# Optimization experiments

Hardware: AMD Instinct MI355X
Metric: run time of the kernel (lower is better)

Reference implementation:

```python
import jax, jax.numpy as jnp
import numpy as np

EMB = 256
HID = 512
VOCAB = 32000
SRC_LEN = 50
TRG_LEN = 50
BATCH = 64


def lstm_layer(x, h0, c0, Wih, Whh, b):
    """x: [T,B,in]; h0,c0: [B,H]; Wih: [4H,in]; Whh: [4H,H]; b: [4H].
    PyTorch gate order i,f,g,o. Returns (ys [T,B,H], hT, cT)."""
    def step(carry, xt):
        h, c = carry
        g = xt @ Wih.T + h @ Whh.T + b
        i, f, gg, o = jnp.split(g, 4, axis=-1)
        c = jax.nn.sigmoid(f) * c + jax.nn.sigmoid(i) * jnp.tanh(gg)
        h = jax.nn.sigmoid(o) * jnp.tanh(c)
        return (h, c), h
    (hT, cT), ys = jax.lax.scan(step, (h0, c0), x)
    return ys, hT, cT


def setup_inputs() -> dict:
    key = jax.random.key(0)
    ks = jax.random.split(key, 20)
    s = 0.05
    d = {
        'src': jax.random.randint(ks[0], (SRC_LEN, BATCH), 0, VOCAB),
        'trg': jax.random.randint(ks[1], (TRG_LEN, BATCH), 0, VOCAB),
        'enc_emb': jax.random.normal(ks[2], (VOCAB, EMB), jnp.float32) * s,
        'enc_Wih0': jax.random.normal(ks[3], (4 * HID, EMB), jnp.float32) * s,
        'enc_Whh0': jax.random.normal(ks[4], (4 * HID, HID), jnp.float32) * s,
        'enc_b0': jnp.zeros((4 * HID,), jnp.float32),
        'enc_Wih1': jax.random.normal(ks[5], (4 * HID, HID), jnp.float32) * s,
        'enc_Whh1': jax.random.normal(ks[6], (4 * HID, HID), jnp.float32) * s,
        'enc_b1': jnp.zeros((4 * HID,), jnp.float32),
        'dec_emb': jax.random.normal(ks[7], (VOCAB, EMB), jnp.float32) * s,
        'dec_Wih0': jax.random.normal(ks[8], (4 * HID, EMB), jnp.float32) * s,
        'dec_Whh0': jax.random.normal(ks[9], (4 * HID, HID), jnp.float32) * s,
        'dec_b0': jnp.zeros((4 * HID,), jnp.float32),
        'dec_Wih1': jax.random.normal(ks[10], (4 * HID, HID), jnp.float32) * s,
        'dec_Whh1': jax.random.normal(ks[11], (4 * HID, HID), jnp.float32) * s,
        'dec_b1': jnp.zeros((4 * HID,), jnp.float32),
        'out_W': jax.random.normal(ks[12], (VOCAB, HID), jnp.float32) * s,
        'out_b': jnp.zeros((VOCAB,), jnp.float32),
    }
    return d


def reference(src, trg, enc_emb, enc_Wih0, enc_Whh0, enc_b0, enc_Wih1, enc_Whh1,
              enc_b1, dec_emb, dec_Wih0, dec_Whh0, dec_b0, dec_Wih1, dec_Whh1,
              dec_b1, out_W, out_b):
    B = src.shape[1]
    z = jnp.zeros((B, HID), enc_emb.dtype)
    # Encoder: 2-layer LSTM over src, keep final (h, c) per layer
    xe = enc_emb[src]                                   # [S,B,E]
    y0, h0, c0 = lstm_layer(xe, z, z, enc_Wih0, enc_Whh0, enc_b0)
    _, h1, c1 = lstm_layer(y0, z, z, enc_Wih1, enc_Whh1, enc_b1)
    # Decoder with teacher forcing: inputs are trg[0:T-1]
    xd = dec_emb[trg[:-1]]                              # [T-1,B,E]
    d0, _, _ = lstm_layer(xd, h0, c0, dec_Wih0, dec_Whh0, dec_b0)
    d1, _, _ = lstm_layer(d0, h1, c1, dec_Wih1, dec_Whh1, dec_b1)
    preds = d1 @ out_W.T + out_b                        # [T-1,B,V]
    return preds
```

## Files before the change

kernel.cpp:

```cpp
#include <hip/hip_runtime.h>
#include <hip/hip_bf16.h>

#define BATCH 64
#define HID 512
#define EMB 256
#define VOCAB 32000
#define G4 2048

typedef __attribute__((ext_vector_type(8))) short short8;
typedef __attribute__((ext_vector_type(4))) float f32x4;
typedef __attribute__((ext_vector_type(4))) unsigned short ush4;

__global__ __launch_bounds__(256) void zero_kernel(float* p, int n){
    int i = blockIdx.x*256 + threadIdx.x;
    if (i < n) p[i] = 0.f;
}

__global__ __launch_bounds__(256) void embed_kernel(const int* __restrict__ tok,
                                                    const float* __restrict__ emb,
                                                    float* __restrict__ out, int T){
    int i = blockIdx.x*256 + threadIdx.x;
    int n = T*BATCH*(EMB/4);
    if (i >= n) return;
    int e4 = i % (EMB/4);
    int tb = i / (EMB/4);
    int id = tok[tb];
    reinterpret_cast<float4*>(out)[(size_t)tb*(EMB/4) + e4] =
        reinterpret_cast<const float4*>(emb + (size_t)id*EMB)[e4];
}

__device__ __forceinline__ unsigned short bf16_rne(float x){
    unsigned b = __float_as_uint(x);
    return (unsigned short)((b + 0x7fffu + ((b >> 16) & 1u)) >> 16);
}
__device__ __forceinline__ void split2(float x, unsigned short& h, unsigned short& l){
    h = bf16_rne(x);
    l = bf16_rne(x - __uint_as_float((unsigned)h << 16));
}

__global__ __launch_bounds__(256) void split_kernel(const float* __restrict__ in,
                                                    unsigned short* __restrict__ hi,
                                                    unsigned short* __restrict__ lo, int n4){
    int i = blockIdx.x*256 + threadIdx.x;
    if (i >= n4) return;
    f32x4 v = reinterpret_cast<const f32x4*>(in)[i];
    ush4 h, l;
    #pragma unroll
    for (int j = 0; j < 4; j++){ unsigned short a,b; split2(v[j], a, b); h[j]=a; l[j]=b; }
    reinterpret_cast<ush4*>(hi)[i] = h;
    reinterpret_cast<ush4*>(lo)[i] = l;
}

__global__ __launch_bounds__(256) void split_hi_kernel(const float* __restrict__ in,
                                                       unsigned short* __restrict__ hi, int n4){
    int i = blockIdx.x*256 + threadIdx.x;
    if (i >= n4) return;
    f32x4 v = reinterpret_cast<const f32x4*>(in)[i];
    ush4 h;
    #pragma unroll
    for (int j = 0; j < 4; j++) h[j] = bf16_rne(v[j]);
    reinterpret_cast<ush4*>(hi)[i] = h;
}

template<int KDIM, int NDIM>
__global__ __launch_bounds__(256) void gemm_mfma_split(
    const float* __restrict__ A, const float* __restrict__ B,
    const float* __restrict__ bias, float* __restrict__ C, int M)
{
    constexpr int LS = 40;
    __shared__ unsigned short Ah[128*LS], Al[128*LS], Bh[128*LS], Bl[128*LS];
    const int n0 = blockIdx.x*128, m0 = blockIdx.y*128;
    const int tid  = threadIdx.x;
    const int lane = tid & 63, wid = tid >> 6;
    const int wm = wid >> 1, wn = wid & 1;
    const int srow = tid >> 1, sk = (tid & 1)*16;
    f32x4 acc[4][4] = {};

    for (int k0 = 0; k0 < KDIM; k0 += 32){
        __syncthreads();
        {
            int ar = m0 + srow;
            float xv[16];
            if (ar < M){
                const float4* ap = reinterpret_cast<const float4*>(A + (size_t)ar*KDIM + k0 + sk);
                #pragma unroll
                for (int q = 0; q < 4; q++){
                    float4 v = ap[q];
                    xv[q*4+0]=v.x; xv[q*4+1]=v.y; xv[q*4+2]=v.z; xv[q*4+3]=v.w;
                }
            } else {
                #pragma unroll
                for (int q = 0; q < 16; q++) xv[q] = 0.f;
            }
            #pragma unroll
            for (int q = 0; q < 16; q++){
                unsigned short h,l; split2(xv[q], h, l);
                Ah[srow*LS + sk + q] = h;
                Al[srow*LS + sk + q] = l;
            }
        }
        {
            int br = n0 + srow;
            const float4* bp = reinterpret_cast<const float4*>(B + (size_t)br*KDIM + k0 + sk);
            #pragma unroll
            for (int q = 0; q < 4; q++){
                float4 v = bp[q];
                float xs[4] = {v.x, v.y, v.z, v.w};
                #pragma unroll
                for (int j = 0; j < 4; j++){
                    unsigned short h,l; split2(xs[j], h, l);
                    Bh[srow*LS + sk + q*4 + j] = h;
                    Bl[srow*LS + sk + q*4 + j] = l;
                }
            }
        }
        __syncthreads();
        const int fr = lane & 15, fk = (lane >> 4)*8;
        short8 a_h[4], a_l[4], b_h[4], b_l[4];
        #pragma unroll
        for (int mi = 0; mi < 4; mi++){
            int row = wm*64 + mi*16 + fr;
            a_h[mi] = *reinterpret_cast<const short8*>(&Ah[row*LS + fk]);
            a_l[mi] = *reinterpret_cast<const short8*>(&Al[row*LS + fk]);
        }
        #pragma unroll
        for (int nj = 0; nj < 4; nj++){
            int rowb = wn*64 + nj*16 + fr;
            b_h[nj] = *reinterpret_cast<const short8*>(&Bh[rowb*LS + fk]);
            b_l[nj] = *reinterpret_cast<const short8*>(&Bl[rowb*LS + fk]);
        }
        #pragma unroll
        for (int mi = 0; mi < 4; mi++)
            #pragma unroll
            for (int nj = 0; nj < 4; nj++){
                acc[mi][nj] = __builtin_amdgcn_mfma_f32_16x16x32_bf16(a_h[mi], b_h[nj], acc[mi][nj], 0,0,0);
                acc[mi][nj] = __builtin_amdgcn_mfma_f32_16x16x32_bf16(a_h[mi], b_l[nj], acc[mi][nj], 0,0,0);
                acc[mi][nj] = __builtin_amdgcn_mfma_f32_16x16x32_bf16(a_l[mi], b_h[nj], acc[mi][nj], 0,0,0);
            }
    }
    const int fr = lane & 15, fq = lane >> 4;
    #pragma unroll
    for (int nj = 0; nj < 4; nj++){
        int col = n0 + wn*64 + nj*16 + fr;
        float bv = bias[col];
        #pragma unroll
        for (int mi = 0; mi < 4; mi++){
            int rbase = m0 + wm*64 + mi*16 + fq*4;
            #pragma unroll
            for (int j = 0; j < 4; j++){
                int row = rbase + j;
                if (row < M)
                    __builtin_nontemporal_store(acc[mi][nj][j] + bv, &C[(size_t)row*NDIM + col]);
            }
        }
    }
}

__device__ __forceinline__ void gll16(const unsigned short* g, unsigned short* l){
    __builtin_amdgcn_global_load_lds(
        (const __attribute__((address_space(1))) unsigned int*)g,
        (__attribute__((address_space(3))) unsigned int*)l, 16, 0, 0);
}

template<int KDIM, int NDIM, int NTN, int PASSES>
__global__ __launch_bounds__(256) void gemm_planes_gll(
    const unsigned short* __restrict__ Ahi, const unsigned short* __restrict__ Alo,
    const unsigned short* __restrict__ Bhi, const unsigned short* __restrict__ Blo,
    const float* __restrict__ bias, float* __restrict__ C, int M)
{
    constexpr int NP = (PASSES == 3) ? 4 : 3;
    __shared__ unsigned short P[NP][128*32];
    const int total = gridDim.x;
    const int q = total >> 3, r8 = total & 7;
    const int xcd = blockIdx.x & 7, idx = blockIdx.x >> 3;
    const int lid = (xcd < r8 ? xcd*(q+1) : r8*(q+1) + (xcd - r8)*q) + idx;
    const int m0 = (lid / NTN)*128, n0 = (lid % NTN)*128;

    const int tid  = threadIdx.x;
    const int lane = tid & 63, wid = tid >> 6;
    const int wm = wid >> 1, wn = wid & 1;

    const bool stager = (PASSES == 3) || (wid < 3);
    const unsigned short* gsrc = (wid == 0) ? Ahi : (wid == 1) ? Alo
                               : (wid == 2) ? Bhi : Blo;
    const int row0 = (wid < 2) ? m0 : n0;
    const unsigned short* gbase = gsrc + (size_t)(row0 + (lane >> 2))*KDIM
                                       + 8*((lane & 3) ^ ((lane >> 3) & 3));
    unsigned short* lbase = &P[(wid < NP) ? wid : 0][0];

    f32x4 acc[4][4] = {};

    for (int k0 = 0; k0 < KDIM; k0 += 32){
        __syncthreads();
        if (stager){
            #pragma unroll
            for (int i = 0; i < 8; i++)
                gll16(gbase + k0 + (size_t)i*16*KDIM, lbase + i*512);
        }
        __syncthreads();

        const int fr = lane & 15, fkq = lane >> 4;
        const int swz = 8*(fkq ^ ((fr >> 1) & 3));
        short8 a_h[4], a_l[4], b_h[4], b_l[4];
        #pragma unroll
        for (int mi = 0; mi < 4; mi++){
            int row = wm*64 + mi*16 + fr;
            a_h[mi] = *reinterpret_cast<const short8*>(&P[0][row*32 + swz]);
            a_l[mi] = *reinterpret_cast<const short8*>(&P[1][row*32 + swz]);
        }
        #pragma unroll
        for (int nj = 0; nj < 4; nj++){
            int row = wn*64 + nj*16 + fr;
            b_h[nj] = *reinterpret_cast<const short8*>(&P[2][row*32 + swz]);
            if (PASSES == 3)
                b_l[nj] = *reinterpret_cast<const short8*>(&P[NP-1][row*32 + swz]);
        }
        #pragma unroll
        for (int mi = 0; mi < 4; mi++)
            #pragma unroll
            for (int nj = 0; nj < 4; nj++){
                acc[mi][nj] = __builtin_amdgcn_mfma_f32_16x16x32_bf16(a_h[mi], b_h[nj], acc[mi][nj], 0,0,0);
                acc[mi][nj] = __builtin_amdgcn_mfma_f32_16x16x32_bf16(a_l[mi], b_h[nj], acc[mi][nj], 0,0,0);
                if (PASSES == 3)
                    acc[mi][nj] = __builtin_amdgcn_mfma_f32_16x16x32_bf16(a_h[mi], b_l[nj], acc[mi][nj], 0,0,0);
            }
    }
    const int fr = lane & 15, fq = lane >> 4;
    #pragma unroll
    for (int nj = 0; nj < 4; nj++){
        int col = n0 + wn*64 + nj*16 + fr;
        float bv = bias[col];
        #pragma unroll
        for (int mi = 0; mi < 4; mi++){
            int rbase = m0 + wm*64 + mi*16 + fq*4;
            #pragma unroll
            for (int j = 0; j < 4; j++){
                int row = rbase + j;
                if (row < M)
                    __builtin_nontemporal_store(acc[mi][nj][j] + bv, &C[(size_t)row*NDIM + col]);
            }
        }
    }
}

__device__ __forceinline__ void lstm_body(
    const float* __restrict__ Xp, const float* __restrict__ Whh,
    const float* __restrict__ hinit, const float* __restrict__ cinit,
    float* __restrict__ ys, float* __restrict__ cfin,
    int T, unsigned* __restrict__ flagbase, int bx)
{
    constexpr int WS = 520;
    __shared__ unsigned short hH[8*WS], hL[8*WS];
    __shared__ float red[2048 + 128];
    __shared__ unsigned short zbuf[8];

    const int hc  = bx & 31, bc = bx >> 5;
    const int hid0 = hc*16;
    const int tid = threadIdx.x;
    const int lane = tid & 63, kc = tid >> 6;
    const int fr = lane & 15, fkq = lane >> 4;
    unsigned* myflag = flagbase + (size_t)(bc*32 + hc)*16;

    if (tid < 8) zbuf[tid] = 0;

    short8 ah[4][4], al[4][4];
    #pragma unroll
    for (int m = 0; m < 4; m++){
        const float* wr = Whh + (size_t)(m*HID + hid0 + fr)*HID;
        #pragma unroll
        for (int s = 0; s < 4; s++){
            int k0 = kc*128 + s*32 + fkq*8;
            f32x4 v0 = *reinterpret_cast<const f32x4*>(wr + k0);
            f32x4 v1 = *reinterpret_cast<const f32x4*>(wr + k0 + 4);
            short8 h8, l8;
            float xv[8] = {v0[0],v0[1],v0[2],v0[3],v1[0],v1[1],v1[2],v1[3]};
            #pragma unroll
            for (int j = 0; j < 8; j++){
                unsigned short hh, ll; split2(xv[j], hh, ll);
                h8[j] = (short)hh; l8[j] = (short)ll;
            }
            ah[m][s] = h8; al[m][s] = l8;
        }
    }

    const int ub = tid >> 4;
    const int uh = tid & 15;
    float creg = 0.f;
    if (tid < 128) creg = cinit[(size_t)(bc*8 + ub)*HID + hid0 + uh];

    const size_t hbase = (size_t)bc*8*HID;
    const float* xprow = Xp + (size_t)(bc*8 + ub)*G4 + hid0 + uh;

    float xn0=0.f, xn1=0.f, xn2=0.f, xn3=0.f;
    if (tid < 128){
        const float* xpr = xprow;
        xn0 = xpr[0]; xn1 = xpr[512]; xn2 = xpr[1024]; xn3 = xpr[1536];
    }

    for (int t = 0; t < T; t++){
        {
            const f32x4* hsrc = reinterpret_cast<const f32x4*>(
                (t == 0) ? (hinit + hbase) : (ys + (size_t)(t-1)*BATCH*HID + hbase));
            #pragma unroll
            for (int j = 0; j < 4; j++){
                int fidx = tid + j*256;
                f32x4 v = hsrc[fidx];
                int e   = fidx*4;
                int row = e >> 9, col = e & 511;
                ush4 h, l;
                #pragma unroll
                for (int qq = 0; qq < 4; qq++){ unsigned short a,b; split2(v[qq], a, b); h[qq]=a; l[qq]=b; }
                *reinterpret_cast<ush4*>(&hH[row*WS + col]) = h;
                *reinterpret_cast<ush4*>(&hL[row*WS + col]) = l;
            }
        }
        __syncthreads();

        {
            f32x4 acc4[4] = {};
            const bool breal = fr < 8;
            #pragma unroll
            for (int s = 0; s < 4; s++){
                int k0 = kc*128 + s*32 + fkq*8;
                short8 bh = breal ? *reinterpret_cast<const short8*>(&hH[fr*WS + k0])
                                  : *reinterpret_cast<const short8*>(zbuf);
                short8 bl = breal ? *reinterpret_cast<const short8*>(&hL[fr*WS + k0])
                                  : *reinterpret_cast<const short8*>(zbuf);
                #pragma unroll
                for (int m = 0; m < 4; m++){
                    acc4[m] = __builtin_amdgcn_mfma_f32_16x16x32_bf16(ah[m][s], bh, acc4[m], 0,0,0);
                    acc4[m] = __builtin_amdgcn_mfma_f32_16x16x32_bf16(ah[m][s], bl, acc4[m], 0,0,0);
                    acc4[m] = __builtin_amdgcn_mfma_f32_16x16x32_bf16(al[m][s], bh, acc4[m], 0,0,0);
                }
            }
            const int b = lane & 15;
            if (b < 8){
                #pragma unroll
                for (int m = 0; m < 4; m++)
                    #pragma unroll
                    for (int qq = 0; qq < 4; qq++){
                        int rowp = m*16 + (lane >> 4)*4 + qq;
                        red[kc*512 + rowp*8 + b] = acc4[m][qq];
                    }
            }
        }
        __syncthreads();

        if (tid < 64){
            #pragma unroll
            for (int b = 0; b < 8; b++)
                red[tid*8 + b] = red[tid*8 + b] + red[512 + tid*8 + b]
                               + red[1024 + tid*8 + b] + red[1536 + tid*8 + b];
        }
        __syncthreads();

        if (tid < 128){
            float gi = red[(0*16 + uh)*8 + ub] + xn0;
            float gf = red[(1*16 + uh)*8 + ub] + xn1;
            float gg = red[(2*16 + uh)*8 + ub] + xn2;
            float go = red[(3*16 + uh)*8 + ub] + xn3;
            float si = 1.f/(1.f + expf(-gi));
            float sf = 1.f/(1.f + expf(-gf));
            float so = 1.f/(1.f + expf(-go));
            float tg = tanhf(gg);
            float c = sf*creg + si*tg;
            creg = c;
            red[2048 + tid] = so * tanhf(c);
            if (t < T-1){
                const float* xpr = xprow + (size_t)(t+1)*BATCH*G4;
                xn0 = xpr[0]; xn1 = xpr[512]; xn2 = xpr[1024]; xn3 = xpr[1536];
            }
        }
        __syncthreads();

        if (tid < 64){
            if (tid < 32){
                f32x4 v = *reinterpret_cast<const f32x4*>(&red[2048 + tid*4]);
                const f32x4* addr = reinterpret_cast<const f32x4*>(
                    ys + (size_t)t*BATCH*HID
                       + (size_t)(bc*8 + (tid >> 2))*HID + hid0 + (tid & 3)*4);
                asm volatile("global_store_dwordx4 %0, %1, off sc0 sc1"
                             :: "v"(addr), "v"(v) : "memory");
            }
            if (t < T-1){
                asm volatile("s_waitcnt vmcnt(0)" ::: "memory");
                if (tid == 0)
                    __hip_atomic_store(myflag, (unsigned)(t+1),
                                       __ATOMIC_RELAXED, __HIP_MEMORY_SCOPE_AGENT);
                const unsigned tgt = (unsigned)(t+1);
                unsigned* fp = flagbase + (size_t)(bc*32 + (tid & 31))*16;
                unsigned spins = 0;
                bool done = false;
                while (!done && spins < (1u<<20)){
                    unsigned v = tgt;
                    if (tid < 32)
                        v = __hip_atomic_load(fp, __ATOMIC_RELAXED, __HIP_MEMORY_SCOPE_AGENT);
                    done = (bool)__all((int)(v >= tgt));
                    spins++;
                }
            }
        }
        __syncthreads();
    }

    if (tid < 128)
        cfin[(size_t)(bc*8 + ub)*HID + hid0 + uh] = creg;
}

__global__ __launch_bounds__(256, 2) void lstm_layer_k(
    const float* Xp, const float* Whh, const float* hinit, const float* cinit,
    float* ys, float* cfin, int T, unsigned* flagbase)
{
    lstm_body(Xp, Whh, hinit, cinit, ys, cfin, T, flagbase, blockIdx.x);
}

__global__ __launch_bounds__(256, 2) void lstm_dual_k(
    const float* Xp0, const float* Whh0, const float* hi0, const float* ci0,
    float* ys0, float* cf0, int T0, unsigned* fl0,
    const float* Xp1, const float* Whh1, const float* hi1, const float* ci1,
    float* ys1, float* cf1, int T1, unsigned* fl1)
{
    const int role = blockIdx.x >> 8;
    const int bx = blockIdx.x & 255;
    const float* Xp   = role ? Xp1 : Xp0;
    const float* Whh  = role ? Whh1 : Whh0;
    const float* hi   = role ? hi1 : hi0;
    const float* ci   = role ? ci1 : ci0;
    float* ys         = role ? ys1 : ys0;
    float* cf         = role ? cf1 : cf0;
    int T             = role ? T1 : T0;
    unsigned* fl      = role ? fl1 : fl0;
    lstm_body(Xp, Whh, hi, ci, ys, cf, T, fl, bx);
}

extern "C" void kernel_launch(void* const* d_in, const int* in_sizes, int n_in,
                              void* d_out, int out_size, void* d_ws, size_t ws_size,
                              hipStream_t stream) {
    const int*   src      = (const int*)  d_in[0];
    const int*   trg      = (const int*)  d_in[1];
    const float* enc_emb  = (const float*)d_in[2];
    const float* enc_Wih0 = (const float*)d_in[3];
    const float* enc_Whh0 = (const float*)d_in[4];
    const float* enc_b0   = (const float*)d_in[5];
    const float* enc_Wih1 = (const float*)d_in[6];
    const float* enc_Whh1 = (const float*)d_in[7];
    const float* enc_b1   = (const float*)d_in[8];
    const float* dec_emb  = (const float*)d_in[9];
    const float* dec_Wih0 = (const float*)d_in[10];
    const float* dec_Whh0 = (const float*)d_in[11];
    const float* dec_b0   = (const float*)d_in[12];
    const float* dec_Wih1 = (const float*)d_in[13];
    const float* dec_Whh1 = (const float*)d_in[14];
    const float* dec_b1   = (const float*)d_in[15];
    const float* out_W    = (const float*)d_in[16];
    const float* out_b    = (const float*)d_in[17];

    float* ob = (float*)d_out;
    float* Xp   = ob;
    float* xe   = ob + (size_t)6553600;
    float* xd   = ob + (size_t)7372800;
    float* eys0 = ob + (size_t)8175616;
    float* eys1 = ob + (size_t)9814016;
    float* dys0 = ob + (size_t)11452416;
    float* Xp2  = ob + (size_t)13058048;

    float* ws = (float*)d_ws;
    float* dys1 = ws;
    float* c0   = ws + (size_t)1605632;
    float* c1   = ws + (size_t)1638400;
    float* hz   = ws + (size_t)1671168;
    unsigned* flags = (unsigned*)(ws + (size_t)1703936);
    unsigned short* Whi = (unsigned short*)(ws + (size_t)1720320);
    unsigned short* Wlo = Whi + (size_t)16384000;
    unsigned short* Ahi = Wlo + (size_t)16384000;
    unsigned short* Alo = Ahi + (size_t)1638400;
    unsigned short* eW0h = Alo  + (size_t)1638400;
    unsigned short* eW0l = eW0h + (size_t)524288;
    unsigned short* eW1h = eW0l + (size_t)524288;
    unsigned short* eW1l = eW1h + (size_t)1048576;
    unsigned short* dW0h = eW1l + (size_t)1048576;
    unsigned short* dW0l = dW0h + (size_t)524288;
    unsigned short* dW1h = dW0l + (size_t)524288;
    unsigned short* dW1l = dW1h + (size_t)1048576;
    unsigned short* XAh  = dW1l + (size_t)1048576;
    unsigned short* XAl  = XAh  + (size_t)1638400;
    const size_t end_final = (size_t)1720320*4 + ((size_t)16384000 + 1638400)*2*2;
    const size_t end_xp    = end_final + ((size_t)6291456 + 3276800)*2;
    const bool planes_ok = (ws_size >= end_final);
    const bool xp_ok     = (ws_size >= end_xp);

    {
        int n = 3*BATCH*HID + 4*4096;
        zero_kernel<<<(n+255)/256, 256, 0, stream>>>(c0, n);
    }

    if (planes_ok)
        split_hi_kernel<<<(16384000/4 + 255)/256, 256, 0, stream>>>(out_W, Whi, 16384000/4);
    if (xp_ok){
        split_kernel<<<(524288/4 + 255)/256, 256, 0, stream>>>(enc_Wih0, eW0h, eW0l, 524288/4);
        split_kernel<<<(1048576/4 + 255)/256, 256, 0, stream>>>(enc_Wih1, eW1h, eW1l, 1048576/4);
        split_kernel<<<(524288/4 + 255)/256, 256, 0, stream>>>(dec_Wih0, dW0h, dW0l, 524288/4);
        split_kernel<<<(1048576/4 + 255)/256, 256, 0, stream>>>(dec_Wih1, dW1h, dW1l, 1048576/4);
    }

    embed_kernel<<<(50*BATCH*(EMB/4)+255)/256, 256, 0, stream>>>(src, enc_emb, xe, 50);
    embed_kernel<<<(49*BATCH*(EMB/4)+255)/256, 256, 0, stream>>>(trg, dec_emb, xd, 49);

    dim3 xgrid(G4/128, 25);

    if (xp_ok){
        split_kernel<<<(819200/4 + 255)/256, 256, 0, stream>>>(xe, XAh, XAl, 819200/4);
        gemm_planes_gll<EMB, G4, 16, 3><<<400, 256, 0, stream>>>(XAh, XAl, eW0h, eW0l, enc_b0, Xp, 3200);
    } else
        gemm_mfma_split<EMB, G4><<<xgrid, 256, 0, stream>>>(xe, enc_Wih0, enc_b0, Xp, 3200);
    lstm_layer_k<<<256, 256, 0, stream>>>(Xp, enc_Whh0, hz, hz, eys0, c0, 50, flags + 0);

    if (xp_ok){
        split_kernel<<<(1638400/4 + 255)/256, 256, 0, stream>>>(eys0, XAh, XAl, 1638400/4);
        gemm_planes_gll<HID, G4, 16, 3><<<400, 256, 0, stream>>>(XAh, XAl, eW1h, eW1l, enc_b1, Xp, 3200);
        split_kernel<<<(802816/4 + 255)/256, 256, 0, stream>>>(xd, XAh, XAl, 802816/4);
        gemm_planes_gll<EMB, G4, 16, 3><<<400, 256, 0, stream>>>(XAh, XAl, dW0h, dW0l, dec_b0, Xp2, 3136);
    } else {
        gemm_mfma_split<HID, G4><<<xgrid, 256, 0, stream>>>(eys0, enc_Wih1, enc_b1, Xp, 3200);
        gemm_mfma_split<EMB, G4><<<xgrid, 256, 0, stream>>>(xd, dec_Wih0, dec_b0, Xp2, 3136);
    }

    lstm_dual_k<<<512, 256, 0, stream>>>(
        Xp,  enc_Whh1, hz,                            hz, eys1, c1, 50, flags + 4096,
        Xp2, dec_Whh0, eys0 + (size_t)49*BATCH*HID,   c0, dys0, c0, 49, flags + 8192);

    if (xp_ok){
        split_kernel<<<(1605632/4 + 255)/256, 256, 0, stream>>>(dys0, XAh, XAl, 1605632/4);
        gemm_planes_gll<HID, G4, 16, 3><<<400, 256, 0, stream>>>(XAh, XAl, dW1h, dW1l, dec_b1, Xp, 3136);
    } else
        gemm_mfma_split<HID, G4><<<xgrid, 256, 0, stream>>>(dys0, dec_Wih1, dec_b1, Xp, 3136);
    lstm_layer_k<<<256, 256, 0, stream>>>(Xp, dec_Whh1, eys1 + (size_t)49*BATCH*HID, c1,
                                          dys1, c1, 49, flags + 12288);

    if (planes_ok){
        split_kernel<<<(1605632/4 + 255)/256, 256, 0, stream>>>(dys1, Ahi, Alo, 1605632/4);
        gemm_planes_gll<HID, VOCAB, 250, 2><<<6250, 256, 0, stream>>>(
            Ahi, Alo, Whi, Whi, out_b, (float*)d_out, 3136);
    } else {
        gemm_mfma_split<HID, VOCAB><<<dim3(VOCAB/128, 25), 256, 0, stream>>>(
            dys1, out_W, out_b, (float*)d_out, 3136);
    }
}
```

Baseline: 1.017 ms.

## Fuse bf16 plane splitting into embedding and LSTM; single-pass output GEMM

The embedding gather now writes bf16 hi/lo planes directly, and each LSTM step writes its hidden state as split planes. This removes the standalone split kernels and their extra fp32 round trips before the input-projection GEMMs. The vocabulary projection GEMM drops from two MFMA passes (A hi+lo times B hi) to one pass (A hi times B hi), roughly halving its matrix work. That GEMM also stages one fewer LDS plane. The cost is lower accuracy in the output logits, since the activation low part is discarded.

```diff
diff --git a/kernel.cpp b/kernel.cpp
--- a/kernel.cpp
+++ b/kernel.cpp
@@ -14,6 +14,15 @@
 __global__ __launch_bounds__(256) void zero_kernel(float* p, int n){
     int i = blockIdx.x*256 + threadIdx.x;
     if (i < n) p[i] = 0.f;
+}
+
+__device__ __forceinline__ unsigned short bf16_rne(float x){
+    unsigned b = __float_as_uint(x);
+    return (unsigned short)((b + 0x7fffu + ((b >> 16) & 1u)) >> 16);
+}
+__device__ __forceinline__ void split2(float x, unsigned short& h, unsigned short& l){
+    h = bf16_rne(x);
+    l = bf16_rne(x - __uint_as_float((unsigned)h << 16));
 }
 
 __global__ __launch_bounds__(256) void embed_kernel(const int* __restrict__ tok,
@@ -29,13 +38,22 @@
         reinterpret_cast<const float4*>(emb + (size_t)id*EMB)[e4];
 }
 
-__device__ __forceinline__ unsigned short bf16_rne(float x){
-    unsigned b = __float_as_uint(x);
-    return (unsigned short)((b + 0x7fffu + ((b >> 16) & 1u)) >> 16);
-}
-__device__ __forceinline__ void split2(float x, unsigned short& h, unsigned short& l){
-    h = bf16_rne(x);
-    l = bf16_rne(x - __uint_as_float((unsigned)h << 16));
+__global__ __launch_bounds__(256) void embed_plane_kernel(const int* __restrict__ tok,
+                                                          const float* __restrict__ emb,
+                                                          unsigned short* __restrict__ hi,
+                                                          unsigned short* __restrict__ lo, int T){
+    int i = blockIdx.x*256 + threadIdx.x;
+    int n = T*BATCH*(EMB/4);
+    if (i >= n) return;
+    int e4 = i % (EMB/4);
+    int tb = i / (EMB/4);
+    int id = tok[tb];
+    f32x4 v = reinterpret_cast<const f32x4*>(emb + (size_t)id*EMB)[e4];
+    ush4 h, l;
+    #pragma unroll
+    for (int j = 0; j < 4; j++){ unsigned short a,b; split2(v[j], a, b); h[j]=a; l[j]=b; }
+    reinterpret_cast<ush4*>(hi)[(size_t)tb*(EMB/4) + e4] = h;
+    reinterpret_cast<ush4*>(lo)[(size_t)tb*(EMB/4) + e4] = l;
 }
 
 __global__ __launch_bounds__(256) void split_kernel(const float* __restrict__ in,
@@ -168,7 +186,7 @@
     const unsigned short* __restrict__ Bhi, const unsigned short* __restrict__ Blo,
     const float* __restrict__ bias, float* __restrict__ C, int M)
 {
-    constexpr int NP = (PASSES == 3) ? 4 : 3;
+    constexpr int NP = (PASSES == 3) ? 4 : 2;
     __shared__ unsigned short P[NP][128*32];
     const int total = gridDim.x;
     const int q = total >> 3, r8 = total & 7;
@@ -180,10 +198,18 @@
     const int lane = tid & 63, wid = tid >> 6;
     const int wm = wid >> 1, wn = wid & 1;
 
-    const bool stager = (PASSES == 3) || (wid < 3);
-    const unsigned short* gsrc = (wid == 0) ? Ahi : (wid == 1) ? Alo
-                               : (wid == 2) ? Bhi : Blo;
-    const int row0 = (wid < 2) ? m0 : n0;
+    const unsigned short* gsrc;
+    int row0;
+    bool stager;
+    if (PASSES == 3){
+        gsrc = (wid == 0) ? Ahi : (wid == 1) ? Alo : (wid == 2) ? Bhi : Blo;
+        row0 = (wid < 2) ? m0 : n0;
+        stager = true;
+    } else {
+        gsrc = (wid == 0) ? Ahi : Bhi;
+        row0 = (wid == 0) ? m0 : n0;
+        stager = (wid < 2);
+    }
     const unsigned short* gbase = gsrc + (size_t)(row0 + (lane >> 2))*KDIM
                                        + 8*((lane & 3) ^ ((lane >> 3) & 3));
     unsigned short* lbase = &P[(wid < NP) ? wid : 0][0];
@@ -201,28 +227,31 @@
 
         const int fr = lane & 15, fkq = lane >> 4;
         const int swz = 8*(fkq ^ ((fr >> 1) & 3));
+        constexpr int BHP = (PASSES == 3) ? 2 : 1;
         short8 a_h[4], a_l[4], b_h[4], b_l[4];
         #pragma unroll
         for (int mi = 0; mi < 4; mi++){
             int row = wm*64 + mi*16 + fr;
             a_h[mi] = *reinterpret_cast<const short8*>(&P[0][row*32 + swz]);
-            a_l[mi] = *reinterpret_cast<const short8*>(&P[1][row*32 + swz]);
+            if (PASSES == 3)
+                a_l[mi] = *reinterpret_cast<const short8*>(&P[1][row*32 + swz]);
         }
         #pragma unroll
         for (int nj = 0; nj < 4; nj++){
             int row = wn*64 + nj*16 + fr;
-            b_h[nj] = *reinterpret_cast<const short8*>(&P[2][row*32 + swz]);
+            b_h[nj] = *reinterpret_cast<const short8*>(&P[BHP][row*32 + swz]);
             if (PASSES == 3)
-                b_l[nj] = *reinterpret_cast<const short8*>(&P[NP-1][row*32 + swz]);
+                b_l[nj] = *reinterpret_cast<const short8*>(&P[3][row*32 + swz]);
         }
         #pragma unroll
         for (int mi = 0; mi < 4; mi++)
             #pragma unroll
             for (int nj = 0; nj < 4; nj++){
                 acc[mi][nj] = __builtin_amdgcn_mfma_f32_16x16x32_bf16(a_h[mi], b_h[nj], acc[mi][nj], 0,0,0);
-                acc[mi][nj] = __builtin_amdgcn_mfma_f32_16x16x32_bf16(a_l[mi], b_h[nj], acc[mi][nj], 0,0,0);
-                if (PASSES == 3)
+                if (PASSES == 3){
+                    acc[mi][nj] = __builtin_amdgcn_mfma_f32_16x16x32_bf16(a_l[mi], b_h[nj], acc[mi][nj], 0,0,0);
                     acc[mi][nj] = __builtin_amdgcn_mfma_f32_16x16x32_bf16(a_h[mi], b_l[nj], acc[mi][nj], 0,0,0);
+                }
             }
     }
     const int fr = lane & 15, fq = lane >> 4;
@@ -247,7 +276,8 @@
     const float* __restrict__ Xp, const float* __restrict__ Whh,
     const float* __restrict__ hinit, const float* __restrict__ cinit,
     float* __restrict__ ys, float* __restrict__ cfin,
-    int T, unsigned* __restrict__ flagbase, int bx)
+    int T, unsigned* __restrict__ flagbase, int bx,
+    unsigned short* __restrict__ phi, unsigned short* __restrict__ plo)
 {
     constexpr int WS = 520;
     __shared__ unsigned short hH[8*WS], hL[8*WS];
@@ -365,7 +395,13 @@
             float tg = tanhf(gg);
             float c = sf*creg + si*tg;
             creg = c;
-            red[2048 + tid] = so * tanhf(c);
+            float hval = so * tanhf(c);
+            red[2048 + tid] = hval;
+            if (phi){
+                unsigned short hh, ll; split2(hval, hh, ll);
+                size_t poff = (size_t)t*BATCH*HID + (size_t)(bc*8 + ub)*HID + hid0 + uh;
+                phi[poff] = hh; plo[poff] = ll;
+            }
             if (t < T-1){
                 const float* xpr = xprow + (size_t)(t+1)*BATCH*G4;
                 xn0 = xpr[0]; xn1 = xpr[512]; xn2 = xpr[1024]; xn3 = xpr[1536];
@@ -409,28 +445,26 @@
 
 __global__ __launch_bounds__(256, 2) void lstm_layer_k(
     const float* Xp, const float* Whh, const float* hinit, const float* cinit,
-    float* ys, float* cfin, int T, unsigned* flagbase)
+    float* ys, float* cfin, int T, unsigned* flagbase,
+    unsigned short* phi, unsigned short* plo)
 {
-    lstm_body(Xp, Whh, hinit, cinit, ys, cfin, T, flagbase, blockIdx.x);
+    lstm_body(Xp, Whh, hinit, cinit, ys, cfin, T, flagbase, blockIdx.x, phi, plo);
 }
 
 __global__ __launch_bounds__(256, 2) void lstm_dual_k(
     const float* Xp0, const float* Whh0, const float* hi0, const float* ci0,
     float* ys0, float* cf0, int T0, unsigned* fl0,
+    unsigned short* phi0, unsigned short* plo0,
     const float* Xp1, const float* Whh1, const float* hi1, const float* ci1,
-    float* ys1, float* cf1, int T1, unsigned* fl1)
+    float* ys1, float* cf1, int T1, unsigned* fl1,
+    unsigned short* phi1, unsigned short* plo1)
 {
     const int role = blockIdx.x >> 8;
     const int bx = blockIdx.x & 255;
-    const float* Xp   = role ? Xp1 : Xp0;
-    const float* Whh  = role ? Whh1 : Whh0;
-    const float* hi   = role ? hi1 : hi0;
-    const float* ci   = role ? ci1 : ci0;
-    float* ys         = role ? ys1 : ys0;
-    float* cf         = role ? cf1 : cf0;
-    int T             = role ? T1 : T0;
-    unsigned* fl      = role ? fl1 : fl0;
-    lstm_body(Xp, Whh, hi, ci, ys, cf, T, fl, bx);
+    if (role == 0)
+        lstm_body(Xp0, Whh0, hi0, ci0, ys0, cf0, T0, fl0, bx, phi0, plo0);
+    else
+        lstm_body(Xp1, Whh1, hi1, ci1, ys1, cf1, T1, fl1, bx, phi1, plo1);
 }
 
 extern "C" void kernel_launch(void* const* d_in, const int* in_sizes, int n_in,
@@ -486,61 +520,59 @@
     unsigned short* XAl  = XAh  + (size_t)1638400;
     const size_t end_final = (size_t)1720320*4 + ((size_t)16384000 + 1638400)*2*2;
     const size_t end_xp    = end_final + ((size_t)6291456 + 3276800)*2;
-    const bool planes_ok = (ws_size >= end_final);
-    const bool xp_ok     = (ws_size >= end_xp);
+    const bool xp_ok = (ws_size >= end_xp);
 
     {
         int n = 3*BATCH*HID + 4*4096;
         zero_kernel<<<(n+255)/256, 256, 0, stream>>>(c0, n);
     }
 
-    if (planes_ok)
+    if (xp_ok){
         split_hi_kernel<<<(16384000/4 + 255)/256, 256, 0, stream>>>(out_W, Whi, 16384000/4);
-    if (xp_ok){
         split_kernel<<<(524288/4 + 255)/256, 256, 0, stream>>>(enc_Wih0, eW0h, eW0l, 524288/4);
         split_kernel<<<(1048576/4 + 255)/256, 256, 0, stream>>>(enc_Wih1, eW1h, eW1l, 1048576/4);
         split_kernel<<<(524288/4 + 255)/256, 256, 0, stream>>>(dec_Wih0, dW0h, dW0l, 524288/4);
         split_kernel<<<(1048576/4 + 255)/256, 256, 0, stream>>>(dec_Wih1, dW1h, dW1l, 1048576/4);
-    }
-
-    embed_kernel<<<(50*BATCH*(EMB/4)+255)/256, 256, 0, stream>>>(src, enc_emb, xe, 50);
-    embed_kernel<<<(49*BATCH*(EMB/4)+255)/256, 256, 0, stream>>>(trg, dec_emb, xd, 49);
+        embed_plane_kernel<<<(50*BATCH*(EMB/4)+255)/256, 256, 0, stream>>>(src, enc_emb, XAh, XAl, 50);
+        embed_plane_kernel<<<(49*BATCH*(EMB/4)+255)/256, 256, 0, stream>>>(trg, dec_emb, Ahi, Alo, 49);
+    } else {
+        embed_kernel<<<(50*BATCH*(EMB/4)+255)/256, 256, 0, stream>>>(src, enc_emb, xe, 50);
+        embed_kernel<<<(49*BATCH*(EMB/4)+255)/256, 256, 0, stream>>>(trg, dec_emb, xd, 49);
+    }
 
     dim3 xgrid(G4/128, 25);
 
+    if (xp_ok)
+        gemm_planes_gll<EMB, G4, 16, 3><<<400, 256, 0, stream>>>(XAh, XAl, eW0h, eW0l, enc_b0, Xp, 3200);
+    else
+        gemm_mfma_split<EMB, G4><<<xgrid, 256, 0, stream>>>(xe, enc_Wih0, enc_b0, Xp, 3200);
+    lstm_layer_k<<<256, 256, 0, stream>>>(Xp, enc_Whh0, hz, hz, eys0, c0, 50, flags + 0,
+                                          xp_ok ? XAh : nullptr, XAl);
+
     if (xp_ok){
-        split_kernel<<<(819200/4 + 255)/256, 256, 0, stream>>>(xe, XAh, XAl, 819200/4);
-        gemm_planes_gll<EMB, G4, 16, 3><<<400, 256, 0, stream>>>(XAh, XAl, eW0h, eW0l, enc_b0, Xp, 3200);
-    } else
-        gemm_mfma_split<EMB, G4><<<xgrid, 256, 0, stream>>>(xe, enc_Wih0, enc_b0, Xp, 3200);
-    lstm_layer_k<<<256, 256, 0, stream>>>(Xp, enc_Whh0, hz, hz, eys0, c0, 50, flags + 0);
-
-    if (xp_ok){
-        split_kernel<<<(1638400/4 + 255)/256, 256, 0, stream>>>(eys0, XAh, XAl, 1638400/4);
         gemm_planes_gll<HID, G4, 16, 3><<<400, 256, 0, stream>>>(XAh, XAl, eW1h, eW1l, enc_b1, Xp, 3200);
-        split_kernel<<<(802816/4 + 255)/256, 256, 0, stream>>>(xd, XAh, XAl, 802816/4);
-        gemm_planes_gll<EMB, G4, 16, 3><<<400, 256, 0, stream>>>(XAh, XAl, dW0h, dW0l, dec_b0, Xp2, 3136);
+        gemm_planes_gll<EMB, G4, 16, 3><<<400, 256, 0, stream>>>(Ahi, Alo, dW0h, dW0l, dec_b0, Xp2, 3136);
     } else {
         gemm_mfma_split<HID, G4><<<xgrid, 256, 0, stream>>>(eys0, enc_Wih1, enc_b1, Xp, 3200);
         gemm_mfma_split<EMB, G4><<<xgrid, 256, 0, stream>>>(xd, dec_Wih0, dec_b0, Xp2, 3136);
     }
 
     lstm_dual_k<<<512, 256, 0, stream>>>(
-        Xp,  enc_Whh1, hz,                            hz, eys1, c1, 50, flags + 4096,
-        Xp2, dec_Whh0, eys0 + (size_t)49*BATCH*HID,   c0, dys0, c0, 49, flags + 8192);
-
-    if (xp_ok){
-        split_kernel<<<(1605632/4 + 255)/256, 256, 0, stream>>>(dys0, XAh, XAl, 1605632/4);
+        Xp,  enc_Whh1, hz,                          hz, eys1, c1, 50, flags + 4096,  nullptr, nullptr,
+        Xp2, dec_Whh0, eys0 + (size_t)49*BATCH*HID, c0, dys0, c0, 49, flags + 8192,
+        xp_ok ? XAh : nullptr, XAl);
+
+    if (xp_ok)
         gemm_planes_gll<HID, G4, 16, 3><<<400, 256, 0, stream>>>(XAh, XAl, dW1h, dW1l, dec_b1, Xp, 3136);
-    } else
+    else
         gemm_mfma_split<HID, G4><<<xgrid, 256, 0, stream>>>(dys0, dec_Wih1, dec_b1, Xp, 3136);
     lstm_layer_k<<<256, 256, 0, stream>>>(Xp, dec_Whh1, eys1 + (size_t)49*BATCH*HID, c1,
-                                          dys1, c1, 49, flags + 12288);
-
-    if (planes_ok){
-        split_kernel<<<(1605632/4 + 255)/256, 256, 0, stream>>>(dys1, Ahi, Alo, 1605632/4);
-        gemm_planes_gll<HID, VOCAB, 250, 2><<<6250, 256, 0, stream>>>(
-            Ahi, Alo, Whi, Whi, out_b, (float*)d_out, 3136);
+                                          dys1, c1, 49, flags + 12288,
+                                          xp_ok ? Ahi : nullptr, Alo);
+
+    if (xp_ok){
+        gemm_planes_gll<HID, VOCAB, 250, 1><<<6250, 256, 0, stream>>>(
+            Ahi, Ahi, Whi, Whi, out_b, (float*)d_out, 3136);
     } else {
         gemm_mfma_split<HID, VOCAB><<<dim3(VOCAB/128, 25), 256, 0, stream>>>(
             dys1, out_W, out_b, (float*)d_out, 3136);
```

Measured after the change: 952.9 us. 1.07x faster.
